# Performance work log

Hardware: AMD Instinct MI355X
Metric: run time of the kernel (lower is better)

Reference implementation:

```python
import jax, jax.numpy as jnp
import numpy as np

N_NODES = 50000
N_EDGES = 800000
N_EVAL = 500000
D = 96


def _sage_conv(x, edge_index, W_l, W_r, b):
    # PyG SAGEConv with aggr='add':
    #   aggr_out[v] = sum_{(u->v) in edges} x[u]
    #   out = aggr_out @ W_l^T-equivalent + b + x @ W_r  (we store W as [in, out])
    src, dst = edge_index[0], edge_index[1]
    msgs = x[src]                                        # [E, d_in] irregular gather
    aggr = jax.ops.segment_sum(msgs, dst, num_segments=x.shape[0])  # [N, d_in]
    return aggr @ W_l + b + x @ W_r                      # [N, d_out]


def setup_inputs() -> dict:
    key = jax.random.key(0)
    ks = jax.random.split(key, 8)
    scale = 1.0 / np.sqrt(D)
    Features = jax.random.normal(ks[0], (N_NODES, D), dtype=jnp.float32)
    A = jax.random.randint(ks[1], (2, N_EDGES), 0, N_NODES, dtype=jnp.int64)
    E = jax.random.randint(ks[2], (2, N_EVAL), 0, N_NODES, dtype=jnp.int64)
    W1_l = jax.random.normal(ks[3], (D, D), dtype=jnp.float32) * scale
    W1_r = jax.random.normal(ks[4], (D, D), dtype=jnp.float32) * scale
    b1 = jnp.zeros((D,), dtype=jnp.float32)
    W2_l = jax.random.normal(ks[5], (D, D), dtype=jnp.float32) * scale
    W2_r = jax.random.normal(ks[6], (D, D), dtype=jnp.float32) * scale
    b2 = jnp.zeros((D,), dtype=jnp.float32)
    return {"Features": Features, "A": A, "E": E,
            "W1_l": W1_l, "W1_r": W1_r, "b1": b1,
            "W2_l": W2_l, "W2_r": W2_r, "b2": b2}


def reference(Features, A, E, W1_l, W1_r, b1, W2_l, W2_r, b2):
    h = _sage_conv(Features, A, W1_l, W1_r, b1)          # [N, hidden]
    h = jax.nn.relu(h)
    # dropout in eval mode = identity
    h = _sage_conv(h, A, W2_l, W2_r, b2)                 # [N, out]
    # edge scoring: gather src/dst embeddings, dot, sigmoid
    src = h[E[0]]                                        # [n_eval, out]
    dst = h[E[1]]                                        # [n_eval, out]
    return jax.nn.sigmoid(jnp.sum(src * dst, axis=-1))   # [n_eval]
```

## Files before the change

kernel.cpp:

```cpp
#include <hip/hip_runtime.h>
#include <math.h>

#define N_NODES 50000
#define N_EDGES 800000
#define N_EVAL  500000
#define CSTRIDE 16
#define MAXDEG  64

__device__ __forceinline__ float4 f4add(float4 a, float4 b) {
    return make_float4(a.x + b.x, a.y + b.y, a.z + b.z, a.w + b.w);
}
__device__ __forceinline__ float4 f4fma(float s, float4 w, float4 a) {
    return make_float4(fmaf(s, w.x, a.x), fmaf(s, w.y, a.y),
                       fmaf(s, w.z, a.z), fmaf(s, w.w, a.w));
}

__global__ __launch_bounds__(256) void k_bucket(const int* __restrict__ src,
                                                const int* __restrict__ dst,
                                                int* __restrict__ degS,
                                                int* __restrict__ bucket) {
    int t = blockIdx.x * 256 + threadIdx.x;
    if (t < N_EDGES / 4) {
        int4 s = ((const int4*)src)[t];
        int4 d = ((const int4*)dst)[t];
        int r0 = atomicAdd(&degS[(size_t)d.x * CSTRIDE], 1);
        int r1 = atomicAdd(&degS[(size_t)d.y * CSTRIDE], 1);
        int r2 = atomicAdd(&degS[(size_t)d.z * CSTRIDE], 1);
        int r3 = atomicAdd(&degS[(size_t)d.w * CSTRIDE], 1);
        if (r0 < MAXDEG) bucket[d.x * MAXDEG + r0] = s.x;
        if (r1 < MAXDEG) bucket[d.y * MAXDEG + r1] = s.y;
        if (r2 < MAXDEG) bucket[d.z * MAXDEG + r2] = s.z;
        if (r3 < MAXDEG) bucket[d.w * MAXDEG + r3] = s.w;
    }
}

__global__ __launch_bounds__(256) void k_aggr(const float* __restrict__ x,
                                              const int* __restrict__ degS,
                                              const int* __restrict__ bucket,
                                              float* __restrict__ out) {
    int gt = blockIdx.x * 256 + threadIdx.x;
    if (gt >= N_NODES * 24) return;
    int v = gt / 24;
    int c = gt - v * 24;
    const float* xp = x + c * 4;
    const int* bk = bucket + v * MAXDEG;
    int deg = degS[(size_t)v * CSTRIDE];
    if (deg > MAXDEG) deg = MAXDEG;
    float4 a0 = make_float4(0.f, 0.f, 0.f, 0.f);
    float4 a1 = make_float4(0.f, 0.f, 0.f, 0.f);
    int i = 0;
    for (; i + 8 <= deg; i += 8) {
        int u0 = bk[i + 0], u1 = bk[i + 1], u2 = bk[i + 2], u3 = bk[i + 3];
        int u4 = bk[i + 4], u5 = bk[i + 5], u6 = bk[i + 6], u7 = bk[i + 7];
        float4 t0 = *(const float4*)(xp + (size_t)u0 * 96);
        float4 t1 = *(const float4*)(xp + (size_t)u1 * 96);
        float4 t2 = *(const float4*)(xp + (size_t)u2 * 96);
        float4 t3 = *(const float4*)(xp + (size_t)u3 * 96);
        float4 t4 = *(const float4*)(xp + (size_t)u4 * 96);
        float4 t5 = *(const float4*)(xp + (size_t)u5 * 96);
        float4 t6 = *(const float4*)(xp + (size_t)u6 * 96);
        float4 t7 = *(const float4*)(xp + (size_t)u7 * 96);
        a0 = f4add(a0, f4add(f4add(t0, t2), f4add(t4, t6)));
        a1 = f4add(a1, f4add(f4add(t1, t3), f4add(t5, t7)));
    }
    for (; i < deg; ++i) {
        int u = bk[i];
        a0 = f4add(a0, *(const float4*)(xp + (size_t)u * 96));
    }
    *(float4*)(out + (size_t)v * 96 + c * 4) = f4add(a0, a1);
}

template <int RELU>
__global__ __launch_bounds__(192) void k_gemm(const float* __restrict__ P,
                                              const float* __restrict__ X,
                                              const float* __restrict__ Wl,
                                              const float* __restrict__ Wr,
                                              const float* __restrict__ bias,
                                              float* __restrict__ out) {
    __shared__ float Ws[32 * 96];
    __shared__ float xT[32 * 68];
    const int tid = threadIdx.x;
    const int q   = tid % 24;
    const int rg  = tid / 24;
    const int v0  = blockIdx.x * 64;

    const int  row0 = tid >> 3,         qd0 = tid & 7;
    const int  row1 = (tid + 192) >> 3, qd1 = (tid + 192) & 7;
    const int  row2 = (tid + 384) >> 3, qd2 = (tid + 384) & 7;
    const bool has2 = (tid < 128);
    int sv0 = v0 + row0; if (sv0 >= N_NODES) sv0 = N_NODES - 1;
    int sv1 = v0 + row1; if (sv1 >= N_NODES) sv1 = N_NODES - 1;
    int sv2 = v0 + row2; if (sv2 >= N_NODES) sv2 = N_NODES - 1;

    float4 bv = *(const float4*)(bias + q * 4);
    float4 acc[8];
    #pragma unroll
    for (int r = 0; r < 8; ++r) acc[r] = make_float4(0.f, 0.f, 0.f, 0.f);

    float4 wreg0, wreg1, wreg2, wreg3;
    float4 xreg0, xreg1, xreg2;

    auto load_chunk = [&](int kc) {
        const float* W = (kc < 3 ? Wl : Wr) + (kc % 3) * (32 * 96);
        const float* M = (kc < 3 ? P : X);
        const int kbase = (kc % 3) * 32;
        wreg0 = *(const float4*)(W + (tid + 0 * 192) * 4);
        wreg1 = *(const float4*)(W + (tid + 1 * 192) * 4);
        wreg2 = *(const float4*)(W + (tid + 2 * 192) * 4);
        wreg3 = *(const float4*)(W + (tid + 3 * 192) * 4);
        xreg0 = *(const float4*)(M + (size_t)sv0 * 96 + kbase + qd0 * 4);
        xreg1 = *(const float4*)(M + (size_t)sv1 * 96 + kbase + qd1 * 4);
        if (has2) xreg2 = *(const float4*)(M + (size_t)sv2 * 96 + kbase + qd2 * 4);
    };
    auto store_chunk = [&]() {
        *(float4*)(Ws + (tid + 0 * 192) * 4) = wreg0;
        *(float4*)(Ws + (tid + 1 * 192) * 4) = wreg1;
        *(float4*)(Ws + (tid + 2 * 192) * 4) = wreg2;
        *(float4*)(Ws + (tid + 3 * 192) * 4) = wreg3;
        int k0 = qd0 * 4;
        xT[(k0 + 0) * 68 + row0] = xreg0.x;
        xT[(k0 + 1) * 68 + row0] = xreg0.y;
        xT[(k0 + 2) * 68 + row0] = xreg0.z;
        xT[(k0 + 3) * 68 + row0] = xreg0.w;
        int k1 = qd1 * 4;
        xT[(k1 + 0) * 68 + row1] = xreg1.x;
        xT[(k1 + 1) * 68 + row1] = xreg1.y;
        xT[(k1 + 2) * 68 + row1] = xreg1.z;
        xT[(k1 + 3) * 68 + row1] = xreg1.w;
        if (has2) {
            int k2 = qd2 * 4;
            xT[(k2 + 0) * 68 + row2] = xreg2.x;
            xT[(k2 + 1) * 68 + row2] = xreg2.y;
            xT[(k2 + 2) * 68 + row2] = xreg2.z;
            xT[(k2 + 3) * 68 + row2] = xreg2.w;
        }
    };

    load_chunk(0);
    for (int kc = 0; kc < 6; ++kc) {
        __syncthreads();
        store_chunk();
        if (kc < 5) load_chunk(kc + 1);
        __syncthreads();
        #pragma unroll 8
        for (int kk = 0; kk < 32; ++kk) {
            float4 w  = *(const float4*)(Ws + kk * 96 + q * 4);
            float4 xa = *(const float4*)(xT + kk * 68 + rg * 8);
            float4 xb = *(const float4*)(xT + kk * 68 + rg * 8 + 4);
            acc[0] = f4fma(xa.x, w, acc[0]);
            acc[1] = f4fma(xa.y, w, acc[1]);
            acc[2] = f4fma(xa.z, w, acc[2]);
            acc[3] = f4fma(xa.w, w, acc[3]);
            acc[4] = f4fma(xb.x, w, acc[4]);
            acc[5] = f4fma(xb.y, w, acc[5]);
            acc[6] = f4fma(xb.z, w, acc[6]);
            acc[7] = f4fma(xb.w, w, acc[7]);
        }
    }
    #pragma unroll
    for (int r = 0; r < 8; ++r) {
        int v = v0 + rg * 8 + r;
        if (v < N_NODES) {
            float4 o = f4add(acc[r], bv);
            if (RELU) {
                o.x = fmaxf(o.x, 0.f); o.y = fmaxf(o.y, 0.f);
                o.z = fmaxf(o.z, 0.f); o.w = fmaxf(o.w, 0.f);
            }
            *(float4*)(out + (size_t)v * 96 + q * 4) = o;
        }
    }
}

__global__ __launch_bounds__(256) void k_score(const float* __restrict__ h,
                                               const int* __restrict__ E,
                                               float* __restrict__ out) {
    int t = blockIdx.x * 256 + threadIdx.x;
    int e = t >> 3, sub = t & 7;
    if (e >= N_EVAL) return;
    int s = E[e];
    int d = E[N_EVAL + e];
    const float* ps = h + (size_t)s * 96 + sub * 12;
    const float* pd = h + (size_t)d * 96 + sub * 12;
    float dot = 0.f;
    #pragma unroll
    for (int i = 0; i < 3; ++i) {
        float4 a = *(const float4*)(ps + i * 4);
        float4 b = *(const float4*)(pd + i * 4);
        dot += a.x * b.x + a.y * b.y + a.z * b.z + a.w * b.w;
    }
    dot += __shfl_xor(dot, 1, 64);
    dot += __shfl_xor(dot, 2, 64);
    dot += __shfl_xor(dot, 4, 64);
    if (sub == 0) out[e] = 1.f / (1.f + expf(-dot));
}


extern "C" void kernel_launch(void* const* d_in, const int* in_sizes, int n_in,
                              void* d_out, int out_size, void* d_ws, size_t ws_size,
                              hipStream_t stream) {
    const float* Features = (const float*)d_in[0];
    const int*   A        = (const int*)d_in[1];
    const int*   E        = (const int*)d_in[2];
    const float* W1l = (const float*)d_in[3];
    const float* W1r = (const float*)d_in[4];
    const float* b1  = (const float*)d_in[5];
    const float* W2l = (const float*)d_in[6];
    const float* W2r = (const float*)d_in[7];
    const float* b2  = (const float*)d_in[8];
    float* out = (float*)d_out;

    char* p = (char*)d_ws;
    auto alloc = [&](size_t bytes) -> char* {
        char* q = p;
        p += (bytes + 255) & ~(size_t)255;
        return q;
    };
    int*   degS   = (int*)alloc((size_t)N_NODES * CSTRIDE * 4);
    int*   bucket = (int*)alloc((size_t)N_NODES * MAXDEG * 4);
    float* bufA   = (float*)alloc((size_t)N_NODES * 96 * 4);
    float* bufB   = (float*)alloc((size_t)N_NODES * 96 * 4);

    const int* Asrc = A;
    const int* Adst = A + N_EDGES;

    hipMemsetAsync(degS, 0, (size_t)N_NODES * CSTRIDE * 4, stream);
    k_bucket<<<(N_EDGES / 4 + 255) / 256, 256, 0, stream>>>(Asrc, Adst, degS, bucket);

    k_aggr<<<(N_NODES * 24 + 255) / 256, 256, 0, stream>>>(Features, degS, bucket, bufA);
    k_gemm<1><<<(N_NODES + 63) / 64, 192, 0, stream>>>(bufA, Features, W1l, W1r, b1, bufB);

    k_aggr<<<(N_NODES * 24 + 255) / 256, 256, 0, stream>>>(bufB, degS, bucket, bufA);
    k_gemm<0><<<(N_NODES + 63) / 64, 192, 0, stream>>>(bufA, bufB, W2l, W2r, b2, bufA);

    k_score<<<(N_EVAL * 8 + 255) / 256, 256, 0, stream>>>(bufA, E, out);
}
```

Measured before the change: 337.8 us.

## Split self-term GEMM and co-schedule it with bucket and aggregation blocks

Each SAGE layer's x@W_r + b term is pulled out into a separate 256-thread GEMM role. That role is placed in the same launch as the bucketing kernel (layer 1) or the neighbor aggregation (layer 2), with blocks interleaved by index. The remaining GEMM only does the aggr@W_l half and adds the precomputed self term from a new buffer. The aim is to overlap compute-bound GEMM blocks with latency-bound atomic and gather blocks and shorten the K loop of the dependent GEMM. The cost is an extra N×96 float buffer that is written and read back, plus more branching inside the fused kernels.

```diff
diff --git a/kernel.cpp b/kernel.cpp
--- a/kernel.cpp
+++ b/kernel.cpp
@@ -6,6 +6,8 @@
 #define N_EVAL  500000
 #define CSTRIDE 16
 #define MAXDEG  64
+#define NB_GEMM ((N_NODES + 63) / 64)
+#define NB_AGG  ((N_NODES * 24 + 255) / 256)
 
 __device__ __forceinline__ float4 f4add(float4 a, float4 b) {
     return make_float4(a.x + b.x, a.y + b.y, a.z + b.z, a.w + b.w);
@@ -15,11 +17,12 @@
                        fmaf(s, w.z, a.z), fmaf(s, w.w, a.w));
 }
 
-__global__ __launch_bounds__(256) void k_bucket(const int* __restrict__ src,
-                                                const int* __restrict__ dst,
-                                                int* __restrict__ degS,
-                                                int* __restrict__ bucket) {
-    int t = blockIdx.x * 256 + threadIdx.x;
+
+__device__ __forceinline__ void bucket_role(int idx, const int* __restrict__ src,
+                                            const int* __restrict__ dst,
+                                            int* __restrict__ degS,
+                                            int* __restrict__ bucket) {
+    int t = idx * 256 + threadIdx.x;
     if (t < N_EDGES / 4) {
         int4 s = ((const int4*)src)[t];
         int4 d = ((const int4*)dst)[t];
@@ -34,11 +37,11 @@
     }
 }
 
-__global__ __launch_bounds__(256) void k_aggr(const float* __restrict__ x,
-                                              const int* __restrict__ degS,
-                                              const int* __restrict__ bucket,
-                                              float* __restrict__ out) {
-    int gt = blockIdx.x * 256 + threadIdx.x;
+__device__ __forceinline__ void aggr_role(int idx, const float* __restrict__ x,
+                                          const int* __restrict__ degS,
+                                          const int* __restrict__ bucket,
+                                          float* __restrict__ out) {
+    int gt = idx * 256 + threadIdx.x;
     if (gt >= N_NODES * 24) return;
     int v = gt / 24;
     int c = gt - v * 24;
@@ -70,13 +73,124 @@
     *(float4*)(out + (size_t)v * 96 + c * 4) = f4add(a0, a1);
 }
 
+__device__ __forceinline__ void selfgemm_role(int g, const float* __restrict__ X,
+                                              const float* __restrict__ W96,
+                                              const float* __restrict__ bias,
+                                              float* __restrict__ S,
+                                              float* __restrict__ Ws,
+                                              float* __restrict__ xT) {
+    const int tid = threadIdx.x;
+    const int j   = tid & 31;
+    const int ty  = tid >> 5;
+    const int v0  = g * 64;
+
+    float acc[8][3];
+    float b0 = bias[j], b1 = bias[j + 32], b2 = bias[j + 64];
+    #pragma unroll
+    for (int r = 0; r < 8; ++r) { acc[r][0] = b0; acc[r][1] = b1; acc[r][2] = b2; }
+
+    const int sr = tid >> 2;
+    const int sc = tid & 3;
+    int sv = v0 + sr; if (sv >= N_NODES) sv = N_NODES - 1;
+
+    for (int kc = 0; kc < 3; ++kc) {
+        const float* W = W96 + kc * (32 * 96);
+        const int kbase = kc * 32;
+        __syncthreads();
+        #pragma unroll
+        for (int i = 0; i < 3; ++i) {
+            int f = tid + i * 256;
+            *(float4*)(Ws + f * 4) = *(const float4*)(W + f * 4);
+        }
+        {
+            const float* rowp = X + (size_t)sv * 96 + kbase;
+            float4 a = *(const float4*)(rowp + sc * 4);
+            float4 b = *(const float4*)(rowp + sc * 4 + 16);
+            int k0 = sc * 4;
+            xT[(k0 + 0) * 68 + sr] = a.x;
+            xT[(k0 + 1) * 68 + sr] = a.y;
+            xT[(k0 + 2) * 68 + sr] = a.z;
+            xT[(k0 + 3) * 68 + sr] = a.w;
+            xT[(k0 + 16) * 68 + sr] = b.x;
+            xT[(k0 + 17) * 68 + sr] = b.y;
+            xT[(k0 + 18) * 68 + sr] = b.z;
+            xT[(k0 + 19) * 68 + sr] = b.w;
+        }
+        __syncthreads();
+        #pragma unroll 8
+        for (int kk = 0; kk < 32; ++kk) {
+            float w0 = Ws[kk * 96 + j];
+            float w1 = Ws[kk * 96 + j + 32];
+            float w2 = Ws[kk * 96 + j + 64];
+            float4 xa = *(const float4*)(xT + kk * 68 + ty * 8);
+            float4 xb = *(const float4*)(xT + kk * 68 + ty * 8 + 4);
+#define ROWFMA(r, xv)                                   \
+            acc[r][0] = fmaf(xv, w0, acc[r][0]);        \
+            acc[r][1] = fmaf(xv, w1, acc[r][1]);        \
+            acc[r][2] = fmaf(xv, w2, acc[r][2]);
+            ROWFMA(0, xa.x) ROWFMA(1, xa.y) ROWFMA(2, xa.z) ROWFMA(3, xa.w)
+            ROWFMA(4, xb.x) ROWFMA(5, xb.y) ROWFMA(6, xb.z) ROWFMA(7, xb.w)
+#undef ROWFMA
+        }
+    }
+    #pragma unroll
+    for (int r = 0; r < 8; ++r) {
+        int v = v0 + ty * 8 + r;
+        if (v < N_NODES) {
+            S[(size_t)v * 96 + j]      = acc[r][0];
+            S[(size_t)v * 96 + j + 32] = acc[r][1];
+            S[(size_t)v * 96 + j + 64] = acc[r][2];
+        }
+    }
+}
+
+
+__global__ __launch_bounds__(256) void k_fusedA(const int* __restrict__ src,
+                                                const int* __restrict__ dst,
+                                                int* __restrict__ degS,
+                                                int* __restrict__ bucket,
+                                                const float* __restrict__ X,
+                                                const float* __restrict__ Wr,
+                                                const float* __restrict__ bias,
+                                                float* __restrict__ S) {
+    __shared__ float Ws[32 * 96];
+    __shared__ float xT[32 * 68];
+    int b = blockIdx.x;
+    if (b & 1) selfgemm_role(b >> 1, X, Wr, bias, S, Ws, xT);
+    else       bucket_role(b >> 1, src, dst, degS, bucket);
+}
+
+__global__ __launch_bounds__(256) void k_aggr(const float* __restrict__ x,
+                                              const int* __restrict__ degS,
+                                              const int* __restrict__ bucket,
+                                              float* __restrict__ out) {
+    aggr_role(blockIdx.x, x, degS, bucket, out);
+}
+
+__global__ __launch_bounds__(256) void k_fusedC(const float* __restrict__ h1,
+                                                const int* __restrict__ degS,
+                                                const int* __restrict__ bucket,
+                                                float* __restrict__ aggrOut,
+                                                const float* __restrict__ Wr,
+                                                const float* __restrict__ bias,
+                                                float* __restrict__ S) {
+    __shared__ float Ws[32 * 96];
+    __shared__ float xT[32 * 68];
+    int b = blockIdx.x;
+    int g = b / 7, r = b % 7;
+    if (r == 3) {
+        if (g < NB_GEMM) selfgemm_role(g, h1, Wr, bias, S, Ws, xT);
+    } else {
+        int idx = g * 6 + (r < 3 ? r : r - 1);
+        if (idx < NB_AGG) aggr_role(idx, h1, degS, bucket, aggrOut);
+    }
+}
+
 template <int RELU>
-__global__ __launch_bounds__(192) void k_gemm(const float* __restrict__ P,
-                                              const float* __restrict__ X,
-                                              const float* __restrict__ Wl,
-                                              const float* __restrict__ Wr,
-                                              const float* __restrict__ bias,
-                                              float* __restrict__ out) {
+__global__ __launch_bounds__(192) void k_gemmH(const float* __restrict__ P,
+                                               const float* __restrict__ Wl,
+                                               const float* __restrict__ S,
+                                               float* __restrict__ out) {
     __shared__ float Ws[32 * 96];
     __shared__ float xT[32 * 68];
     const int tid = threadIdx.x;
@@ -92,7 +206,6 @@
     int sv1 = v0 + row1; if (sv1 >= N_NODES) sv1 = N_NODES - 1;
     int sv2 = v0 + row2; if (sv2 >= N_NODES) sv2 = N_NODES - 1;
 
-    float4 bv = *(const float4*)(bias + q * 4);
     float4 acc[8];
     #pragma unroll
     for (int r = 0; r < 8; ++r) acc[r] = make_float4(0.f, 0.f, 0.f, 0.f);
@@ -101,16 +214,15 @@
     float4 xreg0, xreg1, xreg2;
 
     auto load_chunk = [&](int kc) {
-        const float* W = (kc < 3 ? Wl : Wr) + (kc % 3) * (32 * 96);
-        const float* M = (kc < 3 ? P : X);
-        const int kbase = (kc % 3) * 32;
+        const float* W = Wl + kc * (32 * 96);
+        const int kbase = kc * 32;
         wreg0 = *(const float4*)(W + (tid + 0 * 192) * 4);
         wreg1 = *(const float4*)(W + (tid + 1 * 192) * 4);
         wreg2 = *(const float4*)(W + (tid + 2 * 192) * 4);
         wreg3 = *(const float4*)(W + (tid + 3 * 192) * 4);
-        xreg0 = *(const float4*)(M + (size_t)sv0 * 96 + kbase + qd0 * 4);
-        xreg1 = *(const float4*)(M + (size_t)sv1 * 96 + kbase + qd1 * 4);
-        if (has2) xreg2 = *(const float4*)(M + (size_t)sv2 * 96 + kbase + qd2 * 4);
+        xreg0 = *(const float4*)(P + (size_t)sv0 * 96 + kbase + qd0 * 4);
+        xreg1 = *(const float4*)(P + (size_t)sv1 * 96 + kbase + qd1 * 4);
+        if (has2) xreg2 = *(const float4*)(P + (size_t)sv2 * 96 + kbase + qd2 * 4);
     };
     auto store_chunk = [&]() {
         *(float4*)(Ws + (tid + 0 * 192) * 4) = wreg0;
@@ -137,10 +249,10 @@
     };
 
     load_chunk(0);
-    for (int kc = 0; kc < 6; ++kc) {
+    for (int kc = 0; kc < 3; ++kc) {
         __syncthreads();
         store_chunk();
-        if (kc < 5) load_chunk(kc + 1);
+        if (kc < 2) load_chunk(kc + 1);
         __syncthreads();
         #pragma unroll 8
         for (int kk = 0; kk < 32; ++kk) {
@@ -161,7 +273,8 @@
     for (int r = 0; r < 8; ++r) {
         int v = v0 + rg * 8 + r;
         if (v < N_NODES) {
-            float4 o = f4add(acc[r], bv);
+            float4 s4 = *(const float4*)(S + (size_t)v * 96 + q * 4);
+            float4 o = f4add(acc[r], s4);
             if (RELU) {
                 o.x = fmaxf(o.x, 0.f); o.y = fmaxf(o.y, 0.f);
                 o.z = fmaxf(o.z, 0.f); o.w = fmaxf(o.w, 0.f);
@@ -219,18 +332,19 @@
     int*   bucket = (int*)alloc((size_t)N_NODES * MAXDEG * 4);
     float* bufA   = (float*)alloc((size_t)N_NODES * 96 * 4);
     float* bufB   = (float*)alloc((size_t)N_NODES * 96 * 4);
+    float* bufS   = (float*)alloc((size_t)N_NODES * 96 * 4);
 
     const int* Asrc = A;
     const int* Adst = A + N_EDGES;
 
     hipMemsetAsync(degS, 0, (size_t)N_NODES * CSTRIDE * 4, stream);
-    k_bucket<<<(N_EDGES / 4 + 255) / 256, 256, 0, stream>>>(Asrc, Adst, degS, bucket);
-
-    k_aggr<<<(N_NODES * 24 + 255) / 256, 256, 0, stream>>>(Features, degS, bucket, bufA);
-    k_gemm<1><<<(N_NODES + 63) / 64, 192, 0, stream>>>(bufA, Features, W1l, W1r, b1, bufB);
-
-    k_aggr<<<(N_NODES * 24 + 255) / 256, 256, 0, stream>>>(bufB, degS, bucket, bufA);
-    k_gemm<0><<<(N_NODES + 63) / 64, 192, 0, stream>>>(bufA, bufB, W2l, W2r, b2, bufA);
-
+
+    k_fusedA<<<2 * NB_GEMM, 256, 0, stream>>>(Asrc, Adst, degS, bucket,
+                                              Features, W1r, b1, bufS);
+    k_aggr<<<NB_AGG, 256, 0, stream>>>(Features, degS, bucket, bufA);
+    k_gemmH<1><<<NB_GEMM, 192, 0, stream>>>(bufA, W1l, bufS, bufB);
+    k_fusedC<<<7 * NB_GEMM, 256, 0, stream>>>(bufB, degS, bucket, bufA,
+                                              W2r, b2, bufS);
+    k_gemmH<0><<<NB_GEMM, 192, 0, stream>>>(bufA, W2l, bufS, bufA);
     k_score<<<(N_EVAL * 8 + 255) / 256, 256, 0, stream>>>(bufA, E, out);
 }
```

New measurement: 309.5 us, median of 2. -8.4%, faster.
